# Kernel optimization log

Hardware: AMD Instinct MI355X
Metric: run time of the kernel (lower is better)

## Reference

```python
import jax, jax.numpy as jnp
import numpy as np

B, S, D, DC, H = 4, 2048, 768, 384, 12
HD = DC // H  # compressed head_dim = 32


def setup_inputs() -> dict:
    key = jax.random.key(0)
    ks = jax.random.split(key, 8)
    std = 0.02
    return {
        "hidden_states": jax.random.normal(ks[0], (B, S, D), dtype=jnp.float32),
        "W_attn": jax.random.normal(ks[1], (D, 3 * D), dtype=jnp.float32) * std,
        "b_attn": jnp.zeros((3 * D,), dtype=jnp.float32),
        "P_q": jax.random.normal(ks[2], (D, DC), dtype=jnp.float32) * std,
        "P_k": jax.random.normal(ks[3], (D, DC), dtype=jnp.float32) * std,
        "P_v": jax.random.normal(ks[4], (D, DC), dtype=jnp.float32) * std,
        "W_back": jax.random.normal(ks[5], (DC, D), dtype=jnp.float32) * std,
        "W_proj": jax.random.normal(ks[6], (D, D), dtype=jnp.float32) * std,
        "b_proj": jnp.zeros((D,), dtype=jnp.float32),
    }


def reference(hidden_states, W_attn, b_attn, P_q, P_k, P_v, W_back, W_proj, b_proj):
    b, s, _ = hidden_states.shape
    # GPT-2 Conv1D style c_attn: out = x @ W + b, then split into q,k,v
    qkv = hidden_states @ W_attn + b_attn          # [B,S,3D]
    q, k, v = jnp.split(qkv, 3, axis=-1)           # each [B,S,D]
    # sparsify hooks: per-token linear compression D -> DC
    q = q @ P_q                                    # [B,S,DC]
    k = k @ P_k
    v = v @ P_v
    # split heads -> [B,H,S,HD]
    split = lambda t: t.reshape(b, s, H, HD).transpose(0, 2, 1, 3)
    qh, kh, vh = split(q), split(k), split(v)
    # naive attention with explicit causal mask (as in original _attn)
    scores = jnp.einsum("bhqd,bhkd->bhqk", qh, kh) / jnp.sqrt(jnp.float32(HD))
    causal = jnp.tril(jnp.ones((s, s), dtype=scores.dtype))  # [S,S]
    scores = scores * causal + (-10000.0) * (1.0 - causal)
    weights = jax.nn.softmax(scores, axis=-1)
    ctx = jnp.einsum("bhqk,bhkd->bhqd", weights, vh)         # [B,H,S,HD]
    # merge heads -> [B,S,DC]
    ctx = ctx.transpose(0, 2, 1, 3).reshape(b, s, DC)
    # backproject DC -> D, then c_proj
    out = ctx @ W_back                             # [B,S,D]
    out = out @ W_proj + b_proj                    # [B,S,D]
    return out
```

## Files before the change

kernel.cpp:

```cpp
#include <hip/hip_runtime.h>
#include <math.h>


typedef unsigned short u16;
typedef unsigned int   u32;

#define VLD 8320

using short8 = __attribute__((ext_vector_type(8))) short;
using bf16x4 = __attribute__((ext_vector_type(4))) short;
using f32x4  = __attribute__((ext_vector_type(4))) float;

__device__ __forceinline__ u16 f2bf(float f) {
  u32 u = __builtin_bit_cast(u32, f);
  u = (u + 0x7fffu + ((u >> 16) & 1u)) >> 16;
  return (u16)u;
}

__device__ __forceinline__ float b2f(u16 b) {
  return __builtin_bit_cast(float, (u32)b << 16);
}

__device__ __forceinline__ u32 cvtpk_bf16(float lo, float hi) {
  u32 d;
  asm("v_cvt_pk_bf16_f32 %0, %1, %2" : "=v"(d) : "v"(lo), "v"(hi));
  return d;
}

__device__ __forceinline__ bf16x4 pack4(const f32x4 v) {
  union { u32 u[2]; bf16x4 s; } c;
  c.u[0] = cvtpk_bf16(v[0], v[1]);
  c.u[1] = cvtpk_bf16(v[2], v[3]);
  return c.s;
}

__device__ __forceinline__ float exp2v(float x) {
  return __builtin_amdgcn_exp2f(x);
}

__device__ __forceinline__ f32x4 mfma16bf(bf16x4 a, bf16x4 b, f32x4 c) {
#if __has_builtin(__builtin_amdgcn_mfma_f32_16x16x16bf16_1k)
  return __builtin_amdgcn_mfma_f32_16x16x16bf16_1k(a, b, c, 0, 0, 0);
#elif __has_builtin(__builtin_amdgcn_mfma_f32_16x16x16_bf16)
  return __builtin_amdgcn_mfma_f32_16x16x16_bf16(a, b, c, 0, 0, 0);
#else
  f32x4 d;
  asm("v_mfma_f32_16x16x16_bf16 %0, %1, %2, %3"
      : "=v"(d) : "v"(a), "v"(b), "v"(c));
  return d;
#endif
}

__device__ __forceinline__ void gload_lds16(const void* g, void* l) {
  __builtin_amdgcn_global_load_lds((__attribute__((address_space(1))) u32*)g,
                                   (__attribute__((address_space(3))) u32*)l,
                                   16, 0, 0);
}

__global__ __launch_bounds__(256) void prep_all(
    const float* __restrict__ x, const float* __restrict__ Wa,
    const float* __restrict__ Wb, const float* __restrict__ Pq,
    const float* __restrict__ Pk, const float* __restrict__ Pv,
    const float* __restrict__ Wp,
    u16* __restrict__ x_bf, u16* __restrict__ Wat_bf, u16* __restrict__ Wbk_bf,
    u16* __restrict__ PT, u16* __restrict__ WprT) {
  __shared__ float t[32][33];
  const int blk = blockIdx.x, tid = threadIdx.x;
  if (blk < 8160) {
    const float* src; u16* dst; int i;
    if (blk < 6144)      { src = x;  dst = x_bf;   i = blk * 256 + tid; }
    else if (blk < 7872) { src = Wa; dst = Wat_bf; i = (blk - 6144) * 256 + tid; }
    else                 { src = Wb; dst = Wbk_bf; i = (blk - 7872) * 256 + tid; }
    const float4 v = ((const float4*)src)[i];
    ((ushort4*)dst)[i] = make_ushort4(f2bf(v.x), f2bf(v.y), f2bf(v.z), f2bf(v.w));
    return;
  }
  const float* src; u16* dst; int C, R, bx, by;
  if (blk < 8448)      { src = Pq; dst = PT;             R = 768; C = 384; int t2 = blk - 8160; bx = t2 % 12; by = t2 / 12; }
  else if (blk < 8736) { src = Pk; dst = PT + 384 * 768; R = 768; C = 384; int t2 = blk - 8448; bx = t2 % 12; by = t2 / 12; }
  else if (blk < 9024) { src = Pv; dst = PT + 768 * 768; R = 768; C = 384; int t2 = blk - 8736; bx = t2 % 12; by = t2 / 12; }
  else                 { src = Wp; dst = WprT;           R = 768; C = 768; int t2 = blk - 9024; bx = t2 % 24; by = t2 / 24; }
  const int c0 = bx * 32, r0 = by * 32, tx = tid & 31, ty = tid >> 5;
  for (int i = ty; i < 32; i += 8)
    t[i][tx] = src[(size_t)(r0 + i) * C + c0 + tx];
  __syncthreads();
  for (int i = ty; i < 32; i += 8)
    dst[(size_t)(c0 + i) * R + r0 + tx] = f2bf(t[tx][i]);
}

template<int OBF16>
__device__ __forceinline__ void gemm_tile(
    const u16* __restrict__ A, const u16* __restrict__ BT,
    const float* __restrict__ bias, void* __restrict__ Cv,
    int K, int lda, int ldb, int ldc, int m0, int n0, int biasmode, bool slab,
    u16* As, u16* Bs) {
  const int tid = threadIdx.x;
  const int l = tid & 63, w = tid >> 6;
  const int r = l & 15, g = l >> 4;
  const int koff = slab ? (m0 / 384) * 768 : 0;
  const u16* Ap = A + ((size_t)m0 + w * 16 + r) * lda + g * 8;
  const u16* Bp = BT + ((size_t)n0 + w * 16 + r) * ldb + koff + g * 8;
  f32x4 acc[4][4] = {};
  const int wma = (w >> 1) * 4, wnb = (w & 1) * 4;
  const int nk = K >> 5;

  auto stage = [&](int kt, int buf) {
    const int o = buf * 4096;
    gload_lds16(Ap + kt,                    &As[o + (size_t)tid * 8]);
    gload_lds16(Ap + kt + (size_t)64 * lda, &As[o + 2048 + (size_t)tid * 8]);
    gload_lds16(Bp + kt,                    &Bs[o + (size_t)tid * 8]);
    gload_lds16(Bp + kt + (size_t)64 * ldb, &Bs[o + 2048 + (size_t)tid * 8]);
  };

  stage(0, 0);
  __syncthreads();
  int cur = 0;
  for (int t = 0; t < nk; ++t) {
    if (t + 1 < nk) stage((t + 1) << 5, cur ^ 1);
    const int o = cur * 4096;
    short8 af[4], bfr[4];
    #pragma unroll
    for (int i = 0; i < 4; ++i) {
      af[i]  = *(const short8*)&As[o + ((wma + i) * 64 + l) * 8];
      bfr[i] = *(const short8*)&Bs[o + ((wnb + i) * 64 + l) * 8];
    }
    #pragma unroll
    for (int mi = 0; mi < 4; ++mi)
      #pragma unroll
      for (int ni = 0; ni < 4; ++ni)
        acc[mi][ni] = __builtin_amdgcn_mfma_f32_16x16x32_bf16(af[mi], bfr[ni],
                                                              acc[mi][ni], 0, 0, 0);
    __syncthreads();
    cur ^= 1;
  }

  const int row0 = m0 + (w >> 1) * 64, col0 = n0 + (w & 1) * 64;
  #pragma unroll
  for (int ni = 0; ni < 4; ++ni) {
    const int col = col0 + ni * 16 + r;
    const float bvc = (biasmode == 1) ? bias[col] : 0.f;
    #pragma unroll
    for (int mi = 0; mi < 4; ++mi)
      #pragma unroll
      for (int j = 0; j < 4; ++j) {
        const int row = row0 + mi * 16 + 4 * g + j;
        float bv = bvc;
        if (biasmode == 2) bv = bias[row];
        const float v = acc[mi][ni][j] + bv;
        if (OBF16) ((u16*)Cv)[(size_t)row * ldc + col] = f2bf(v);
        else       ((float*)Cv)[(size_t)row * ldc + col] = v;
      }
  }
}

__global__ __launch_bounds__(256, 2) void gemm_prep(
    const u16* __restrict__ PT, const u16* __restrict__ Wat,
    const u16* __restrict__ WprT, const u16* __restrict__ Wbk,
    const float* __restrict__ ba,
    u16* __restrict__ WcT, u16* __restrict__ WbpT, float* __restrict__ bc) {
  __shared__ alignas(16) u16 As[8192], Bs[8192];
  const int t = blockIdx.x;
  if (t < 54) {
    gemm_tile<1>(PT, Wat, nullptr, WcT, 768, 768, 2304, 768,
                 (t % 9) * 128, (t / 9) * 128, 0, true, As, Bs);
  } else if (t < 72) {
    const int t2 = t - 54;
    gemm_tile<1>(WprT, Wbk, nullptr, WbpT, 768, 768, 768, 384,
                 (t2 % 6) * 128, (t2 / 6) * 128, 0, false, As, Bs);
  } else {
    const int c = (t - 72) * 144 + threadIdx.x;
    if (threadIdx.x < 144 && c < 1152) {
      const int slab = c / 384;
      const float* bs = ba + slab * 768;
      const u16* row = PT + (size_t)c * 768;
      float s = 0.f;
      for (int jj = 0; jj < 96; ++jj) {
        const short8 v = *(const short8*)&row[jj * 8];
        #pragma unroll
        for (int e = 0; e < 8; ++e)
          s = fmaf(bs[jj * 8 + e], b2f((u16)v[e]), s);
      }
      bc[c] = s;
    }
  }
}

__global__ __launch_bounds__(256, 2) void gemm_qkvt(
    const u16* __restrict__ x_bf, const u16* __restrict__ WcT,
    const float* __restrict__ bc, u16* __restrict__ QKbuf, u16* __restrict__ VTbuf) {
  __shared__ alignas(16) u16 As[8192], Bs[8192];
  const int t = blockIdx.x;
  if (t < 384) {
    gemm_tile<1>(x_bf, WcT, bc, QKbuf, 768, 768, 768, 768,
                 (t % 64) * 128, (t / 64) * 128, 1, false, As, Bs);
  } else {
    const int t2 = t - 384;
    gemm_tile<1>(WcT + (size_t)768 * 768, x_bf, bc + 768, VTbuf, 768, 768, 768, VLD,
                 (t2 % 3) * 128, (t2 / 3) * 128, 2, false, As, Bs);
  }
}

__global__ __launch_bounds__(256, 2) void gemm_out(
    const u16* __restrict__ ctx, const u16* __restrict__ WbpT,
    const float* __restrict__ bp, float* __restrict__ out) {
  __shared__ alignas(16) u16 As[8192], Bs[8192];
  const int t = blockIdx.x;
  gemm_tile<0>(ctx, WbpT, bp, out, 384, 384, 384, 768,
               (t % 64) * 128, (t / 64) * 128, 1, false, As, Bs);
}

__global__ __launch_bounds__(512, 1) void attn_kernel(
    const u16* __restrict__ QK, const u16* __restrict__ VT,
    u16* __restrict__ ctx) {
  __shared__ alignas(16) u16 Ks[2][2048];
  __shared__ alignas(16) u16 Vs[2][32 * 72];
  const int tid = threadIdx.x;
  const int w = tid >> 6, l = tid & 63;
  const int r = l & 15, g = l >> 4;
  const int idx = blockIdx.x;
  const int c = 7 - idx / 48;
  const int bh = idx % 48;
  const int b = bh / 12, h = bh % 12;
  const size_t tok0 = (size_t)b * 2048;
  const int q0 = c * 256 + w * 32;
  const u16* Qb = QK + (tok0 + q0) * 768 + h * 32;
  const u16* Kb = QK + tok0 * 768 + 384 + h * 32;
  const u16* Vb = VT + (size_t)(h * 32) * VLD + b * 2048;
  const float scale2 = 0.25500526474f;
  const float THR = 8.0f;
  const f32x4 fz = {0.f, 0.f, 0.f, 0.f};

  short8 qf[2];
  qf[0] = *(const short8*)&Qb[(size_t)r * 768 + 8 * g];
  qf[1] = *(const short8*)&Qb[(size_t)(16 + r) * 768 + 8 * g];

  float mrun[2] = {-3.0e38f, -3.0e38f};
  float lpart[2] = {0.f, 0.f};
  f32x4 o[2][2] = {};
  const int ntb = 4 * (c + 1);
  const int ntw = (q0 + 31) / 64 + 1;

  const int krow = ((tid >> 6) << 4) + (tid & 15);
  const int kcol = ((tid >> 4) & 3) * 8;
  const int vd   = (tid - 256) >> 3;
  const int vkc  = ((tid - 256) & 7) * 8;

  auto stage = [&](int t, int buf) {
    if (tid < 256) {
      gload_lds16(&Kb[(size_t)(t * 64 + krow) * 768 + kcol], &Ks[buf][(size_t)tid * 8]);
    } else {
      const uint4 v = *(const uint4*)&Vb[(size_t)vd * VLD + t * 64 + vkc];
      *(uint4*)&Vs[buf][vd * 72 + vkc] = v;
    }
  };

  stage(0, 0);
  __syncthreads();
  int cur = 0;
  for (int t = 0; t < ntb; ++t) {
    if (t + 1 < ntb) stage(t + 1, cur ^ 1);
    if (t < ntw) {
      short8 kf[4];
      #pragma unroll
      for (int kj = 0; kj < 4; ++kj)
        kf[kj] = *(const short8*)&Ks[cur][((kj * 64 + l)) * 8];
      bf16x4 vf[2][4];
      #pragma unroll
      for (int di = 0; di < 2; ++di)
        #pragma unroll
        for (int kj = 0; kj < 4; ++kj)
          vf[di][kj] = *(const bf16x4*)&Vs[cur][(16 * di + r) * 72 + kj * 16 + 4 * g];

      f32x4 s[2][4];
      __builtin_amdgcn_s_setprio(1);
      #pragma unroll
      for (int kj = 0; kj < 4; ++kj)
        #pragma unroll
        for (int mi = 0; mi < 2; ++mi)
          s[mi][kj] = __builtin_amdgcn_mfma_f32_16x16x32_bf16(kf[kj], qf[mi], fz, 0, 0, 0);
      __builtin_amdgcn_s_setprio(0);

      if (t == ntw - 1) {
        #pragma unroll
        for (int mi = 0; mi < 2; ++mi) {
          const int qq = q0 + mi * 16 + r;
          #pragma unroll
          for (int kj = 0; kj < 4; ++kj)
            #pragma unroll
            for (int jj = 0; jj < 4; ++jj) {
              const int kk = t * 64 + kj * 16 + 4 * g + jj;
              if (kk > qq) s[mi][kj][jj] = -3.0e38f;
            }
        }
      }

      #pragma unroll
      for (int mi = 0; mi < 2; ++mi) {
        const float a0 = fmaxf(fmaxf(s[mi][0][0], s[mi][0][1]), fmaxf(s[mi][0][2], s[mi][0][3]));
        const float a1 = fmaxf(fmaxf(s[mi][1][0], s[mi][1][1]), fmaxf(s[mi][1][2], s[mi][1][3]));
        const float a2 = fmaxf(fmaxf(s[mi][2][0], s[mi][2][1]), fmaxf(s[mi][2][2], s[mi][2][3]));
        const float a3 = fmaxf(fmaxf(s[mi][3][0], s[mi][3][1]), fmaxf(s[mi][3][2], s[mi][3][3]));
        const float lmxs = fmaxf(fmaxf(a0, a1), fmaxf(a2, a3)) * scale2;
        if (__any(lmxs > mrun[mi] + THR)) {
          float mx = lmxs;
          mx = fmaxf(mx, __shfl_xor(mx, 16));
          mx = fmaxf(mx, __shfl_xor(mx, 32));
          const float mnew = fmaxf(mrun[mi], mx);
          const float al = exp2v(mrun[mi] - mnew);
          mrun[mi] = mnew;
          lpart[mi] *= al;
          o[0][mi] *= al;
          o[1][mi] *= al;
        }
        #pragma unroll
        for (int kj = 0; kj < 4; ++kj)
          #pragma unroll
          for (int jj = 0; jj < 4; ++jj) {
            const float pv = exp2v(fmaf(s[mi][kj][jj], scale2, -mrun[mi]));
            s[mi][kj][jj] = pv;
            lpart[mi] += pv;
          }
      }

      __builtin_amdgcn_s_setprio(1);
      #pragma unroll
      for (int kj = 0; kj < 4; ++kj) {
        const bf16x4 pf0 = pack4(s[0][kj]);
        const bf16x4 pf1 = pack4(s[1][kj]);
        #pragma unroll
        for (int di = 0; di < 2; ++di) {
          o[di][0] = mfma16bf(vf[di][kj], pf0, o[di][0]);
          o[di][1] = mfma16bf(vf[di][kj], pf1, o[di][1]);
        }
      }
      __builtin_amdgcn_s_setprio(0);
    }
    __syncthreads();
    cur ^= 1;
  }

  #pragma unroll
  for (int mi = 0; mi < 2; ++mi) {
    float lr = lpart[mi];
    lr += __shfl_xor(lr, 16);
    lr += __shfl_xor(lr, 32);
    const float li = 1.0f / lr;
    const size_t row = tok0 + q0 + mi * 16 + r;
    #pragma unroll
    for (int di = 0; di < 2; ++di) {
      const u32 d0 = cvtpk_bf16(o[di][mi][0] * li, o[di][mi][1] * li);
      const u32 d1 = cvtpk_bf16(o[di][mi][2] * li, o[di][mi][3] * li);
      *(uint2*)&ctx[row * 384 + h * 32 + di * 16 + 4 * g] = make_uint2(d0, d1);
    }
  }
}

extern "C" void kernel_launch(void* const* d_in, const int* in_sizes, int n_in,
                              void* d_out, int out_size, void* d_ws, size_t ws_size,
                              hipStream_t stream) {
  const float* x      = (const float*)d_in[0];
  const float* W_attn = (const float*)d_in[1];
  const float* b_attn = (const float*)d_in[2];
  const float* P_q    = (const float*)d_in[3];
  const float* P_k    = (const float*)d_in[4];
  const float* P_v    = (const float*)d_in[5];
  const float* W_back = (const float*)d_in[6];
  const float* W_proj = (const float*)d_in[7];
  const float* b_proj = (const float*)d_in[8];

  char* ws = (char*)d_ws;
  u16*   x_bf   = (u16*)(ws);
  u16*   ctx    = (u16*)(ws);
  u16*   Wat_bf = (u16*)(ws + 12582912);
  u16*   PT     = (u16*)(ws + 16121856);
  u16*   Wbk_bf = (u16*)(ws + 17891328);
  u16*   WprT   = (u16*)(ws + 18481152);
  u16*   WcT    = (u16*)(ws + 19660800);
  u16*   WbpT   = (u16*)(ws + 21430272);
  float* bc     = (float*)(ws + 22020096);
  u16*   QKbuf  = (u16*)d_out;
  u16*   VTbuf  = (u16*)((char*)d_out + 12582912);
  float* out    = (float*)d_out;

  prep_all<<<9600, 256, 0, stream>>>(x, W_attn, W_back, P_q, P_k, P_v, W_proj,
                                     x_bf, Wat_bf, Wbk_bf, PT, WprT);
  gemm_prep<<<80, 256, 0, stream>>>(PT, Wat_bf, WprT, Wbk_bf, b_attn, WcT, WbpT, bc);
  gemm_qkvt<<<576, 256, 0, stream>>>(x_bf, WcT, bc, QKbuf, VTbuf);
  attn_kernel<<<384, 512, 0, stream>>>(QKbuf, VTbuf, ctx);
  gemm_out<<<384, 256, 0, stream>>>(ctx, WbpT, b_proj, out);
}
```

Baseline: 134.6 us.

## Split attention blocks to 128 queries with 256 threads and register-staged V prefetch

The attention kernel now uses 256-thread blocks, each covering 128 query rows instead of 256, and launches twice as many blocks (768) with launch bounds allowing four blocks per CU. All threads now do both the K async copy and the V load. The V tile is loaded into registers before compute and written to LDS after compute, so the global latency overlaps the MFMA work. This aims at better occupancy and finer causal load balance, at the cost of more redundant K/V tile loads per query and extra register pressure from holding V.

```diff
diff --git a/kernel.cpp b/kernel.cpp
--- a/kernel.cpp
+++ b/kernel.cpp
@@ -209,7 +209,7 @@
                (t % 64) * 128, (t / 64) * 128, 1, false, As, Bs);
 }
 
-__global__ __launch_bounds__(512, 1) void attn_kernel(
+__global__ __launch_bounds__(256, 4) void attn_kernel(
     const u16* __restrict__ QK, const u16* __restrict__ VT,
     u16* __restrict__ ctx) {
   __shared__ alignas(16) u16 Ks[2][2048];
@@ -218,11 +218,11 @@
   const int w = tid >> 6, l = tid & 63;
   const int r = l & 15, g = l >> 4;
   const int idx = blockIdx.x;
-  const int c = 7 - idx / 48;
+  const int cc = 15 - idx / 48;
   const int bh = idx % 48;
   const int b = bh / 12, h = bh % 12;
   const size_t tok0 = (size_t)b * 2048;
-  const int q0 = c * 256 + w * 32;
+  const int q0 = cc * 128 + w * 32;
   const u16* Qb = QK + (tok0 + q0) * 768 + h * 32;
   const u16* Kb = QK + tok0 * 768 + 384 + h * 32;
   const u16* Vb = VT + (size_t)(h * 32) * VLD + b * 2048;
@@ -237,28 +237,31 @@
   float mrun[2] = {-3.0e38f, -3.0e38f};
   float lpart[2] = {0.f, 0.f};
   f32x4 o[2][2] = {};
-  const int ntb = 4 * (c + 1);
+  const int ntb = 2 * (cc + 1);
   const int ntw = (q0 + 31) / 64 + 1;
 
   const int krow = ((tid >> 6) << 4) + (tid & 15);
   const int kcol = ((tid >> 4) & 3) * 8;
-  const int vd   = (tid - 256) >> 3;
-  const int vkc  = ((tid - 256) & 7) * 8;
-
-  auto stage = [&](int t, int buf) {
-    if (tid < 256) {
-      gload_lds16(&Kb[(size_t)(t * 64 + krow) * 768 + kcol], &Ks[buf][(size_t)tid * 8]);
-    } else {
-      const uint4 v = *(const uint4*)&Vb[(size_t)vd * VLD + t * 64 + vkc];
-      *(uint4*)&Vs[buf][vd * 72 + vkc] = v;
-    }
+  const int vd   = tid >> 3;
+  const int vkc  = (tid & 7) * 8;
+
+  uint4 vreg;
+  auto stageK = [&](int t, int buf) {
+    gload_lds16(&Kb[(size_t)(t * 64 + krow) * 768 + kcol], &Ks[buf][(size_t)tid * 8]);
   };
-
-  stage(0, 0);
+  auto loadV = [&](int t) {
+    vreg = *(const uint4*)&Vb[(size_t)vd * VLD + t * 64 + vkc];
+  };
+  auto writeV = [&](int buf) {
+    *(uint4*)&Vs[buf][vd * 72 + vkc] = vreg;
+  };
+
+  loadV(0); stageK(0, 0); writeV(0);
   __syncthreads();
   int cur = 0;
   for (int t = 0; t < ntb; ++t) {
-    if (t + 1 < ntb) stage(t + 1, cur ^ 1);
+    const bool pf = (t + 1 < ntb);
+    if (pf) { loadV(t + 1); stageK(t + 1, cur ^ 1); }
     if (t < ntw) {
       short8 kf[4];
       #pragma unroll
@@ -335,6 +338,7 @@
       }
       __builtin_amdgcn_s_setprio(0);
     }
+    if (pf) writeV(cur ^ 1);
     __syncthreads();
     cur ^= 1;
   }
@@ -386,6 +390,6 @@
                                      x_bf, Wat_bf, Wbk_bf, PT, WprT);
   gemm_prep<<<80, 256, 0, stream>>>(PT, Wat_bf, WprT, Wbk_bf, b_attn, WcT, WbpT, bc);
   gemm_qkvt<<<576, 256, 0, stream>>>(x_bf, WcT, bc, QKbuf, VTbuf);
-  attn_kernel<<<384, 512, 0, stream>>>(QKbuf, VTbuf, ctx);
+  attn_kernel<<<768, 256, 0, stream>>>(QKbuf, VTbuf, ctx);
   gemm_out<<<384, 256, 0, stream>>>(ctx, WbpT, b_proj, out);
 }
```

New measurement: 125.3 us. 1.07x faster.
